# Kernel tuning notes

Measured on AMD Instinct MI355X. Metric: run time of the kernel, lower is better.

Reference implementation:

```python
import jax, jax.numpy as jnp
import numpy as np
import math

B, S, N, F = 512, 72, 5, 10
H, C = 4, 32          # GAT heads, per-head dim
D = H * C             # 128 d_model
L, FF = 3, 256        # transformer layers, ffn dim
K, NS = 6, 5          # horizons, stations
EPS = 1e-5


def layer_norm(x, g, b):
    m = x.mean(-1, keepdims=True)
    v = ((x - m) ** 2).mean(-1, keepdims=True)
    return (x - m) / jnp.sqrt(v + EPS) * g + b


def setup_inputs() -> dict:
    key = jax.random.key(0)
    ks = jax.random.split(key, 16)
    # all 20 directed non-self edges of the 5-node graph
    src, dst = np.nonzero(1 - np.eye(N, dtype=np.int32))
    edge_index = jnp.asarray(np.stack([src, dst]).astype(np.int32))
    w = lambda k, shp: (jax.random.normal(k, shp, jnp.float32) * 0.05)
    return {
        "x": jax.random.normal(ks[0], (B, S, N, F), jnp.float32),
        "edge_index": edge_index,
        "gat_w": w(ks[1], (F, D)),
        "gat_att_src": w(ks[2], (H, C)),
        "gat_att_dst": w(ks[3], (H, C)),
        "gat_bias": jnp.zeros((D,), jnp.float32),
        "gat_ln_g": jnp.ones((D,), jnp.float32),
        "gat_ln_b": jnp.zeros((D,), jnp.float32),
        "qkv_w": w(ks[4], (L, 3 * D, D)),
        "qkv_b": jnp.zeros((L, 3 * D), jnp.float32),
        "out_w": w(ks[5], (L, D, D)),
        "out_b": jnp.zeros((L, D), jnp.float32),
        "ln1_g": jnp.ones((L, D), jnp.float32),
        "ln1_b": jnp.zeros((L, D), jnp.float32),
        "ff1_w": w(ks[6], (L, FF, D)),
        "ff1_b": jnp.zeros((L, FF), jnp.float32),
        "ff2_w": w(ks[7], (L, D, FF)),
        "ff2_b": jnp.zeros((L, D), jnp.float32),
        "ln2_g": jnp.ones((L, D), jnp.float32),
        "ln2_b": jnp.zeros((L, D), jnp.float32),
        "h1_w": w(ks[8], (K, D // 2, D)),
        "h1_b": jnp.zeros((K, D // 2), jnp.float32),
        "h2_w": w(ks[9], (K, NS, D // 2)),
        "h2_b": jnp.zeros((K, NS), jnp.float32),
    }


def reference(x, edge_index, gat_w, gat_att_src, gat_att_dst, gat_bias,
              gat_ln_g, gat_ln_b, qkv_w, qkv_b, out_w, out_b,
              ln1_g, ln1_b, ff1_w, ff1_b, ff2_w, ff2_b, ln2_g, ln2_b,
              h1_w, h1_b, h2_w, h2_b):
    G = B * S                                  # number of independent graphs
    xf = x.reshape(G, N, F)
    # GATConv: per-node projection then edge-softmax attention per destination
    h = jnp.einsum('gnf,fhc->gnhc', xf, gat_w.reshape(F, H, C))   # [G,N,H,C]
    a_src = jnp.einsum('gnhc,hc->gnh', h, gat_att_src)
    a_dst = jnp.einsum('gnhc,hc->gnh', h, gat_att_dst)
    # add self loops (GATConv default; input has no self loops)
    loops = jnp.arange(N, dtype=edge_index.dtype)
    src = jnp.concatenate([edge_index[0], loops])   # [E2]
    dst = jnp.concatenate([edge_index[1], loops])
    e = jax.nn.leaky_relu(a_src[:, src] + a_dst[:, dst], 0.2)     # [G,E2,H]
    et = e.transpose(1, 0, 2)                                     # [E2,G,H]
    m = jax.ops.segment_max(et, dst, num_segments=N)              # [N,G,H]
    ex = jnp.exp(et - m[dst])
    denom = jax.ops.segment_sum(ex, dst, num_segments=N)          # [N,G,H]
    alpha = ex / denom[dst]                                       # [E2,G,H]
    msg = alpha[..., None] * h[:, src].transpose(1, 0, 2, 3)      # [E2,G,H,C]
    agg = jax.ops.segment_sum(msg, dst, num_segments=N)           # [N,G,H,C]
    gat_out = agg.transpose(1, 0, 2, 3).reshape(G, N, D) + gat_bias
    gat_out = layer_norm(gat_out, gat_ln_g, gat_ln_b)

    # mean-pool over nodes -> temporal sequence [B,S,D]
    t = gat_out.reshape(B, S, N, D).mean(axis=2)

    # sinusoidal positional encoding
    pos = jnp.arange(S, dtype=jnp.float32)[:, None]
    div = jnp.exp(jnp.arange(0, D, 2, dtype=jnp.float32) * (-math.log(10000.0) / D))
    pe = jnp.zeros((S, D), jnp.float32)
    pe = pe.at[:, 0::2].set(jnp.sin(pos * div)).at[:, 1::2].set(jnp.cos(pos * div))
    t = t + pe

    scale = 1.0 / math.sqrt(D // H)
    for l in range(L):
        qkv = t @ qkv_w[l].T + qkv_b[l]                 # [B,S,3D]
        q, k, v = jnp.split(qkv, 3, axis=-1)
        q = q.reshape(B, S, H, D // H)
        k = k.reshape(B, S, H, D // H)
        v = v.reshape(B, S, H, D // H)
        scores = jnp.einsum('bqhd,bkhd->bhqk', q, k) * scale
        att = jax.nn.softmax(scores, axis=-1)
        o = jnp.einsum('bhqk,bkhd->bqhd', att, v).reshape(B, S, D)
        o = o @ out_w[l].T + out_b[l]
        t = layer_norm(t + o, ln1_g[l], ln1_b[l])       # post-norm
        f = jax.nn.relu(t @ ff1_w[l].T + ff1_b[l]) @ ff2_w[l].T + ff2_b[l]
        t = layer_norm(t + f, ln2_g[l], ln2_b[l])

    x_last = t[:, -1, :]                                # [B,D]
    h1 = jax.nn.relu(jnp.einsum('bd,kod->kbo', x_last, h1_w) + h1_b[:, None, :])
    out = jnp.einsum('kbo,kpo->kbp', h1, h2_w) + h2_b[:, None, :]
    return out  # [K=6 horizons, B, NS=5]
```

## Files before the change

### kernel.cpp

```cpp
#include <hip/hip_runtime.h>
#include <math.h>

constexpr int B_ = 512, S_ = 72, N_ = 5, F_ = 10;
constexpr int H_ = 4, C_ = 32, D_ = 128;
constexpr int L_ = 3, FF_ = 256;
constexpr int K_ = 6, NS_ = 5;
constexpr int G_ = B_ * S_;
constexpr float EPS_ = 1e-5f;
constexpr int SP_ = 80;
constexpr int KP_ = 96;

typedef short bf16x8 __attribute__((ext_vector_type(8)));
typedef float f32x4 __attribute__((ext_vector_type(4)));

__device__ __forceinline__ short f2bf(float f) {
    unsigned int u = __float_as_uint(f);
    u += 0x7FFFu + ((u >> 16) & 1u);
    return (short)(u >> 16);
}

__global__ __launch_bounds__(128) void pe_kernel(float* __restrict__ pe)
{
    const int s = blockIdx.x;
    const int d = threadIdx.x;
    const float expo = -(float)(d & ~1) * (9.210340371976184f / 128.f);
    const float ang = (float)s * expf(expo);
    pe[s * D_ + d] = (d & 1) ? cosf(ang) : sinf(ang);
}

__global__ __launch_bounds__(128) void gatc_kernel(
    const float* __restrict__ gat_w, const float* __restrict__ att_src,
    const float* __restrict__ att_dst, float* __restrict__ gatc)
{
    const int t = threadIdx.x;
    if (t < 40) {
        const int f = t >> 2, h = t & 3;
        float s = 0.f;
#pragma unroll
        for (int c = 0; c < 32; ++c)
            s = fmaf(gat_w[f * D_ + h * 32 + c], att_src[h * 32 + c], s);
        gatc[t] = s;
    } else if (t < 80) {
        const int f = (t - 40) >> 2, h = (t - 40) & 3;
        float s = 0.f;
#pragma unroll
        for (int c = 0; c < 32; ++c)
            s = fmaf(gat_w[f * D_ + h * 32 + c], att_dst[h * 32 + c], s);
        gatc[t] = s;
    }
}

__global__ __launch_bounds__(128) void gat_kernel(
    const float* __restrict__ x,
    const float* __restrict__ gat_w,
    const float* __restrict__ gatc,
    const float* __restrict__ gat_bias,
    const float* __restrict__ ln_g,
    const float* __restrict__ ln_b,
    const float* __restrict__ pe,
    float* __restrict__ t_out)
{
    const int g = blockIdx.x;
    const int d = threadIdx.x;
    const int s = g % S_;
    const int head = d >> 5;

    __shared__ float xs[N_][F_];
    __shared__ float red[N_][2][2];

    if (d < N_ * F_) xs[d / F_][d % F_] = x[(size_t)g * N_ * F_ + d];
    __syncthreads();

    float wcol[F_], wsrcv[F_], wdstv[F_];
#pragma unroll
    for (int f = 0; f < F_; ++f) {
        wcol[f]  = gat_w[f * D_ + d];
        wsrcv[f] = gatc[f * 4 + head];
        wdstv[f] = gatc[40 + f * 4 + head];
    }

    float hn[N_], a_s[N_], a_d[N_];
#pragma unroll
    for (int n = 0; n < N_; ++n) {
        float acc = 0.f, ss = 0.f, dd = 0.f;
#pragma unroll
        for (int f = 0; f < F_; ++f) {
            const float xv = xs[n][f];
            acc = fmaf(xv, wcol[f], acc);
            ss  = fmaf(xv, wsrcv[f], ss);
            dd  = fmaf(xv, wdstv[f], dd);
        }
        hn[n] = acc; a_s[n] = ss; a_d[n] = dd;
    }

    float y[N_];
#pragma unroll
    for (int n = 0; n < N_; ++n) {
        const float ad = a_d[n];
        float e[N_];
        float mx = -1e30f;
#pragma unroll
        for (int m = 0; m < N_; ++m) {
            float v = a_s[m] + ad;
            v = v > 0.f ? v : 0.2f * v;
            e[m] = v;
            mx = fmaxf(mx, v);
        }
        float den = 0.f;
#pragma unroll
        for (int m = 0; m < N_; ++m) { e[m] = __expf(e[m] - mx); den += e[m]; }
        const float inv = 1.f / den;
        float agg = 0.f;
#pragma unroll
        for (int m = 0; m < N_; ++m) agg = fmaf(e[m] * inv, hn[m], agg);
        y[n] = agg + gat_bias[d];
    }

    const int wave = d >> 6;
#pragma unroll
    for (int n = 0; n < N_; ++n) {
        float sm = y[n];
        float sq = y[n] * y[n];
#pragma unroll
        for (int off = 32; off >= 1; off >>= 1) {
            sm += __shfl_xor(sm, off);
            sq += __shfl_xor(sq, off);
        }
        if ((d & 63) == 0) { red[n][wave][0] = sm; red[n][wave][1] = sq; }
    }
    __syncthreads();

    const float gg = ln_g[d];
    const float bb = ln_b[d];
    float tacc = 0.f;
#pragma unroll
    for (int n = 0; n < N_; ++n) {
        const float sm = red[n][0][0] + red[n][1][0];
        const float sq = red[n][0][1] + red[n][1][1];
        const float mean = sm * (1.f / D_);
        const float var = sq * (1.f / D_) - mean * mean;
        const float rstd = rsqrtf(var + EPS_);
        tacc += (y[n] - mean) * rstd * gg + bb;
    }
    tacc *= (1.f / N_);

    t_out[(size_t)g * D_ + d] = tacc + pe[s * D_ + d];
}

__global__ __launch_bounds__(256) void linear_mfma_kernel(
    const float* __restrict__ A, const float* __restrict__ W,
    const float* __restrict__ bias, float* __restrict__ out,
    int K, int Cout, int relu)
{
    __shared__ short As[64 * 64];
    __shared__ short Ws[64 * 64];

    const int tid = threadIdx.x;
    const int lane = tid & 63;
    const int wid = tid >> 6;
    const int wr = wid >> 1;
    const int wc = wid & 1;
    const int r0 = blockIdx.x * 64;
    const int c0 = blockIdx.y * 64;

    const int st_row = tid >> 3;
    const int st_slot = tid & 7;

    f32x4 acc[2][2] = {};

    for (int kk = 0; kk < K; kk += 64) {
        if (kk) __syncthreads();
#pragma unroll
        for (int it = 0; it < 2; ++it) {
            const int row = st_row + it * 32;
            const int gk = kk + st_slot * 8;
            const int pslot = st_slot ^ (row & 7);
            {
                const float* src = &A[(size_t)(r0 + row) * K + gk];
                const float4 a0 = *reinterpret_cast<const float4*>(src);
                const float4 a1 = *reinterpret_cast<const float4*>(src + 4);
                bf16x8 h;
                h[0] = f2bf(a0.x); h[1] = f2bf(a0.y);
                h[2] = f2bf(a0.z); h[3] = f2bf(a0.w);
                h[4] = f2bf(a1.x); h[5] = f2bf(a1.y);
                h[6] = f2bf(a1.z); h[7] = f2bf(a1.w);
                *reinterpret_cast<bf16x8*>(&As[row * 64 + pslot * 8]) = h;
            }
            {
                const float* src = &W[(size_t)(c0 + row) * K + gk];
                const float4 w0 = *reinterpret_cast<const float4*>(src);
                const float4 w1 = *reinterpret_cast<const float4*>(src + 4);
                bf16x8 h;
                h[0] = f2bf(w0.x); h[1] = f2bf(w0.y);
                h[2] = f2bf(w0.z); h[3] = f2bf(w0.w);
                h[4] = f2bf(w1.x); h[5] = f2bf(w1.y);
                h[6] = f2bf(w1.z); h[7] = f2bf(w1.w);
                *reinterpret_cast<bf16x8*>(&Ws[row * 64 + pslot * 8]) = h;
            }
        }
        __syncthreads();

#pragma unroll
        for (int j = 0; j < 2; ++j) {
            bf16x8 aF[2], bF[2];
#pragma unroll
            for (int m = 0; m < 2; ++m) {
                const int row = wr * 32 + m * 16 + (lane & 15);
                const int slot = j * 4 + (lane >> 4);
                const int pslot = slot ^ (row & 7);
                aF[m] = *reinterpret_cast<const bf16x8*>(&As[row * 64 + pslot * 8]);
            }
#pragma unroll
            for (int n = 0; n < 2; ++n) {
                const int col = wc * 32 + n * 16 + (lane & 15);
                const int slot = j * 4 + (lane >> 4);
                const int pslot = slot ^ (col & 7);
                bF[n] = *reinterpret_cast<const bf16x8*>(&Ws[col * 64 + pslot * 8]);
            }
#pragma unroll
            for (int m = 0; m < 2; ++m)
#pragma unroll
                for (int n = 0; n < 2; ++n)
                    acc[m][n] = __builtin_amdgcn_mfma_f32_16x16x32_bf16(
                        aF[m], bF[n], acc[m][n], 0, 0, 0);
        }
    }

#pragma unroll
    for (int m = 0; m < 2; ++m) {
#pragma unroll
        for (int n = 0; n < 2; ++n) {
            const int col = c0 + wc * 32 + n * 16 + (lane & 15);
            const float bv = bias[col];
#pragma unroll
            for (int j = 0; j < 4; ++j) {
                const int row = r0 + wr * 32 + m * 16 + (lane >> 4) * 4 + j;
                float v = acc[m][n][j] + bv;
                if (relu) v = fmaxf(v, 0.f);
                out[(size_t)row * Cout + col] = v;
            }
        }
    }
}

__global__ __launch_bounds__(256) void linear_ln_kernel(
    const float* __restrict__ A, const float* __restrict__ W,
    const float* __restrict__ bias, float* __restrict__ t,
    const float* __restrict__ lng, const float* __restrict__ lnb,
    int K)
{
    __shared__ short As[64 * 64];
    __shared__ short Ws2[128 * 64];
    __shared__ float red[64][2][2];

    const int tid = threadIdx.x;
    const int lane = tid & 63;
    const int wid = tid >> 6;
    const int wr = wid >> 1;
    const int wc = wid & 1;
    const int c16 = lane & 15;
    const int grp = lane >> 4;
    const int r0 = blockIdx.x * 64;

    const int st_row = tid >> 3;
    const int st_slot = tid & 7;

    f32x4 acc[2][4] = {};

    for (int kk = 0; kk < K; kk += 64) {
        if (kk) __syncthreads();
#pragma unroll
        for (int it = 0; it < 2; ++it) {
            const int row = st_row + it * 32;
            const int gk = kk + st_slot * 8;
            const int pslot = st_slot ^ (row & 7);
            const float* src = &A[(size_t)(r0 + row) * K + gk];
            const float4 a0 = *reinterpret_cast<const float4*>(src);
            const float4 a1 = *reinterpret_cast<const float4*>(src + 4);
            bf16x8 h;
            h[0] = f2bf(a0.x); h[1] = f2bf(a0.y);
            h[2] = f2bf(a0.z); h[3] = f2bf(a0.w);
            h[4] = f2bf(a1.x); h[5] = f2bf(a1.y);
            h[6] = f2bf(a1.z); h[7] = f2bf(a1.w);
            *reinterpret_cast<bf16x8*>(&As[row * 64 + pslot * 8]) = h;
        }
#pragma unroll
        for (int it = 0; it < 4; ++it) {
            const int row = st_row + it * 32;
            const int gk = kk + st_slot * 8;
            const int pslot = st_slot ^ (row & 7);
            const float* src = &W[(size_t)row * K + gk];
            const float4 w0 = *reinterpret_cast<const float4*>(src);
            const float4 w1 = *reinterpret_cast<const float4*>(src + 4);
            bf16x8 h;
            h[0] = f2bf(w0.x); h[1] = f2bf(w0.y);
            h[2] = f2bf(w0.z); h[3] = f2bf(w0.w);
            h[4] = f2bf(w1.x); h[5] = f2bf(w1.y);
            h[6] = f2bf(w1.z); h[7] = f2bf(w1.w);
            *reinterpret_cast<bf16x8*>(&Ws2[row * 64 + pslot * 8]) = h;
        }
        __syncthreads();

#pragma unroll
        for (int j = 0; j < 2; ++j) {
            bf16x8 aF[2], bF[4];
#pragma unroll
            for (int m = 0; m < 2; ++m) {
                const int row = wr * 32 + m * 16 + c16;
                const int slot = j * 4 + grp;
                const int pslot = slot ^ (row & 7);
                aF[m] = *reinterpret_cast<const bf16x8*>(&As[row * 64 + pslot * 8]);
            }
#pragma unroll
            for (int n = 0; n < 4; ++n) {
                const int col = wc * 64 + n * 16 + c16;
                const int slot = j * 4 + grp;
                const int pslot = slot ^ (col & 7);
                bF[n] = *reinterpret_cast<const bf16x8*>(&Ws2[col * 64 + pslot * 8]);
            }
#pragma unroll
            for (int m = 0; m < 2; ++m)
#pragma unroll
                for (int n = 0; n < 4; ++n)
                    acc[m][n] = __builtin_amdgcn_mfma_f32_16x16x32_bf16(
                        aF[m], bF[n], acc[m][n], 0, 0, 0);
        }
    }

#pragma unroll
    for (int m = 0; m < 2; ++m) {
#pragma unroll
        for (int j = 0; j < 4; ++j) {
            const int row = wr * 32 + m * 16 + 4 * grp + j;
            float sm = 0.f, sq = 0.f;
#pragma unroll
            for (int n = 0; n < 4; ++n) {
                const int col = wc * 64 + n * 16 + c16;
                float v = acc[m][n][j] + bias[col]
                        + t[(size_t)(r0 + row) * D_ + col];
                acc[m][n][j] = v;
                sm += v;
                sq += v * v;
            }
#pragma unroll
            for (int off = 8; off >= 1; off >>= 1) {
                sm += __shfl_xor(sm, off);
                sq += __shfl_xor(sq, off);
            }
            if (c16 == 0) { red[row][wc][0] = sm; red[row][wc][1] = sq; }
        }
    }
    __syncthreads();

#pragma unroll
    for (int m = 0; m < 2; ++m) {
#pragma unroll
        for (int j = 0; j < 4; ++j) {
            const int row = wr * 32 + m * 16 + 4 * grp + j;
            const float sm = red[row][0][0] + red[row][1][0];
            const float sq = red[row][0][1] + red[row][1][1];
            const float mean = sm * (1.f / D_);
            const float var = sq * (1.f / D_) - mean * mean;
            const float rstd = rsqrtf(var + EPS_);
#pragma unroll
            for (int n = 0; n < 4; ++n) {
                const int col = wc * 64 + n * 16 + c16;
                t[(size_t)(r0 + row) * D_ + col] =
                    (acc[m][n][j] - mean) * rstd * lng[col] + lnb[col];
            }
        }
    }
}

__global__ __launch_bounds__(256) void attn_mfma_kernel(
    const float* __restrict__ qkv, float* __restrict__ o)
{
    const int bh = blockIdx.x;
    const int b = bh >> 2;
    const int h = bh & 3;

    __shared__ short Qs[SP_ * 32];
    __shared__ short Ks[SP_ * 32];
    __shared__ short VT[32 * KP_];
    __shared__ short Pb[SP_ * KP_];

    const int tid = threadIdx.x;
    const int lane = tid & 63;
    const int wid = tid >> 6;
    const int g = lane >> 4;
    const int c16 = lane & 15;

    const float scale = 0.17677669529663687f;

    for (int idx = tid; idx < S_ * 8; idx += 256) {
        const int i = idx >> 3;
        const int c4 = (idx & 7) * 4;
        const size_t base = ((size_t)(b * S_ + i)) * 384 + h * 32 + c4;
        const float4 q = *reinterpret_cast<const float4*>(&qkv[base]);
        const float4 k = *reinterpret_cast<const float4*>(&qkv[base + 128]);
        const float4 v = *reinterpret_cast<const float4*>(&qkv[base + 256]);
        short4 qh, kh;
        qh.x = f2bf(q.x * scale); qh.y = f2bf(q.y * scale);
        qh.z = f2bf(q.z * scale); qh.w = f2bf(q.w * scale);
        kh.x = f2bf(k.x); kh.y = f2bf(k.y);
        kh.z = f2bf(k.z); kh.w = f2bf(k.w);
        *reinterpret_cast<short4*>(&Qs[i * 32 + c4]) = qh;
        *reinterpret_cast<short4*>(&Ks[i * 32 + c4]) = kh;
        VT[(c4 + 0) * KP_ + i] = f2bf(v.x);
        VT[(c4 + 1) * KP_ + i] = f2bf(v.y);
        VT[(c4 + 2) * KP_ + i] = f2bf(v.z);
        VT[(c4 + 3) * KP_ + i] = f2bf(v.w);
    }
    for (int idx = tid; idx < 8 * 32; idx += 256) {
        Qs[S_ * 32 + idx] = 0;
        Ks[S_ * 32 + idx] = 0;
    }
    for (int idx = tid; idx < 32 * 24; idx += 256) {
        VT[(idx / 24) * KP_ + 72 + idx % 24] = 0;
    }
    for (int idx = tid; idx < SP_ * 24; idx += 256) {
        Pb[(idx / 24) * KP_ + 72 + idx % 24] = 0;
    }
    __syncthreads();

    float invr[2][4];
#pragma unroll
    for (int mi = 0; mi < 2; ++mi) {
        const int m = wid + 4 * mi;
        if (m <= 4) {
            const int rowb = m * 16;
            const bf16x8 aF = *reinterpret_cast<const bf16x8*>(
                &Qs[(rowb + c16) * 32 + 8 * g]);
            f32x4 sc[5];
#pragma unroll
            for (int n = 0; n < 5; ++n) {
                const bf16x8 bF = *reinterpret_cast<const bf16x8*>(
                    &Ks[(n * 16 + c16) * 32 + 8 * g]);
                f32x4 z = {};
                sc[n] = __builtin_amdgcn_mfma_f32_16x16x32_bf16(aF, bF, z, 0, 0, 0);
            }
#pragma unroll
            for (int j = 0; j < 4; ++j) {
                float mx = -1e30f;
#pragma unroll
                for (int n = 0; n < 5; ++n) {
                    const int col = n * 16 + c16;
                    if (col < S_) mx = fmaxf(mx, sc[n][j]);
                }
                mx = fmaxf(mx, __shfl_xor(mx, 1));
                mx = fmaxf(mx, __shfl_xor(mx, 2));
                mx = fmaxf(mx, __shfl_xor(mx, 4));
                mx = fmaxf(mx, __shfl_xor(mx, 8));
                float den = 0.f;
                float p[5];
#pragma unroll
                for (int n = 0; n < 5; ++n) {
                    const int col = n * 16 + c16;
                    p[n] = (col < S_) ? __expf(sc[n][j] - mx) : 0.f;
                    den += p[n];
                }
                den += __shfl_xor(den, 1);
                den += __shfl_xor(den, 2);
                den += __shfl_xor(den, 4);
                den += __shfl_xor(den, 8);
                invr[mi][j] = 1.f / den;
                const int row = rowb + 4 * g + j;
#pragma unroll
                for (int n = 0; n < 5; ++n)
                    Pb[row * KP_ + n * 16 + c16] = f2bf(p[n]);
            }
        }
    }
    __syncthreads();

#pragma unroll
    for (int mi = 0; mi < 2; ++mi) {
        const int m = wid + 4 * mi;
        if (m <= 4) {
            const int rowb = m * 16;
            f32x4 accO[2] = {};
#pragma unroll
            for (int kk = 0; kk < 3; ++kk) {
                const bf16x8 aF = *reinterpret_cast<const bf16x8*>(
                    &Pb[(rowb + c16) * KP_ + kk * 32 + 8 * g]);
#pragma unroll
                for (int n2 = 0; n2 < 2; ++n2) {
                    const bf16x8 bF = *reinterpret_cast<const bf16x8*>(
                        &VT[(n2 * 16 + c16) * KP_ + kk * 32 + 8 * g]);
                    accO[n2] = __builtin_amdgcn_mfma_f32_16x16x32_bf16(
                        aF, bF, accO[n2], 0, 0, 0);
                }
            }
#pragma unroll
            for (int j = 0; j < 4; ++j) {
                const int row = rowb + 4 * g + j;
                if (row < S_) {
                    const float inv = invr[mi][j];
#pragma unroll
                    for (int n2 = 0; n2 < 2; ++n2) {
                        o[((size_t)(b * S_ + row)) * D_ + h * 32 + n2 * 16 + c16]
                            = accO[n2][j] * inv;
                    }
                }
            }
        }
    }
}

__global__ __launch_bounds__(64) void head_kernel(
    const float* __restrict__ t, const float* __restrict__ h1_w,
    const float* __restrict__ h1_b, const float* __restrict__ h2_w,
    const float* __restrict__ h2_b, float* __restrict__ out)
{
    const int kb = blockIdx.x;
    const int k = kb / B_;
    const int b = kb - k * B_;
    const int o = threadIdx.x;

    const float* xr = &t[((size_t)(b * S_ + S_ - 1)) * D_];
    const float* wr = &h1_w[((size_t)k * 64 + o) * D_];
    float acc = h1_b[k * 64 + o];
#pragma unroll 8
    for (int d = 0; d < D_; ++d) acc = fmaf(xr[d], wr[d], acc);
    const float h1v = fmaxf(acc, 0.f);

#pragma unroll
    for (int p = 0; p < NS_; ++p) {
        float partial = h1v * h2_w[((size_t)k * NS_ + p) * 64 + o];
#pragma unroll
        for (int off = 32; off >= 1; off >>= 1) partial += __shfl_xor(partial, off);
        if (o == 0) out[((size_t)k * B_ + b) * NS_ + p] = partial + h2_b[k * NS_ + p];
    }
}

extern "C" void kernel_launch(void* const* d_in, const int* in_sizes, int n_in,
                              void* d_out, int out_size, void* d_ws, size_t ws_size,
                              hipStream_t stream) {
    const float* x        = (const float*)d_in[0];
    const float* gat_w    = (const float*)d_in[2];
    const float* att_src  = (const float*)d_in[3];
    const float* att_dst  = (const float*)d_in[4];
    const float* gat_bias = (const float*)d_in[5];
    const float* gat_ln_g = (const float*)d_in[6];
    const float* gat_ln_b = (const float*)d_in[7];
    const float* qkv_w    = (const float*)d_in[8];
    const float* qkv_b    = (const float*)d_in[9];
    const float* out_w    = (const float*)d_in[10];
    const float* out_b    = (const float*)d_in[11];
    const float* ln1_g    = (const float*)d_in[12];
    const float* ln1_b    = (const float*)d_in[13];
    const float* ff1_w    = (const float*)d_in[14];
    const float* ff1_b    = (const float*)d_in[15];
    const float* ff2_w    = (const float*)d_in[16];
    const float* ff2_b    = (const float*)d_in[17];
    const float* ln2_g    = (const float*)d_in[18];
    const float* ln2_b    = (const float*)d_in[19];
    const float* h1_w     = (const float*)d_in[20];
    const float* h1_b     = (const float*)d_in[21];
    const float* h2_w     = (const float*)d_in[22];
    const float* h2_b     = (const float*)d_in[23];
    float* out = (float*)d_out;

    float* ws   = (float*)d_ws;
    float* t    = ws;
    float* qkv  = t + (size_t)G_ * D_;
    float* fbuf = qkv + (size_t)G_ * 384;
    float* pe   = fbuf + (size_t)G_ * FF_;
    float* gatc = pe + (size_t)S_ * D_;

    pe_kernel<<<S_, 128, 0, stream>>>(pe);
    gatc_kernel<<<1, 128, 0, stream>>>(gat_w, att_src, att_dst, gatc);
    gat_kernel<<<G_, 128, 0, stream>>>(x, gat_w, gatc,
                                       gat_bias, gat_ln_g, gat_ln_b, pe, t);

    for (int l = 0; l < L_; ++l) {
        linear_mfma_kernel<<<dim3(G_ / 64, 384 / 64), 256, 0, stream>>>(
            t, qkv_w + (size_t)l * 384 * D_, qkv_b + (size_t)l * 384, qkv,
            D_, 384, 0);
        attn_mfma_kernel<<<B_ * H_, 256, 0, stream>>>(qkv, fbuf);
        linear_ln_kernel<<<G_ / 64, 256, 0, stream>>>(
            fbuf, out_w + (size_t)l * D_ * D_, out_b + (size_t)l * D_, t,
            ln1_g + l * D_, ln1_b + l * D_, D_);
        linear_mfma_kernel<<<dim3(G_ / 64, FF_ / 64), 256, 0, stream>>>(
            t, ff1_w + (size_t)l * FF_ * D_, ff1_b + (size_t)l * FF_, fbuf,
            D_, FF_, 1);
        linear_ln_kernel<<<G_ / 64, 256, 0, stream>>>(
            fbuf, ff2_w + (size_t)l * D_ * FF_, ff2_b + (size_t)l * D_, t,
            ln2_g + l * D_, ln2_b + l * D_, FF_);
    }

    head_kernel<<<K_ * B_, 64, 0, stream>>>(t, h1_w, h1_b, h2_w, h2_b, out);
}
```

Baseline: 470.2 us.

## Store intermediate activations and weights in bf16 to halve memory traffic

Weights are converted to bf16 once per call in a new kernel, and every intermediate activation buffer (qkv, attention output, ffn hidden, plus a bf16 shadow of t) is written in bf16. The GEMM and attention kernels then load bf16 directly instead of loading fp32 and converting per tile. This cuts global memory traffic and conversion ALU work across all layers. It adds an extra bf16 write of t after each layernorm, and rounding now happens before the bias and scale are applied, which slightly changes numerics.

```diff
diff --git a/kernel.cpp b/kernel.cpp
--- a/kernel.cpp
+++ b/kernel.cpp
@@ -10,6 +10,12 @@
 constexpr int SP_ = 80;
 constexpr int KP_ = 96;
 
+constexpr int WQKV_ = 0;
+constexpr int WOUT_ = 147456;
+constexpr int WFF1_ = 196608;
+constexpr int WFF2_ = 294912;
+constexpr int WTOT_ = 393216;
+
 typedef short bf16x8 __attribute__((ext_vector_type(8)));
 typedef float f32x4 __attribute__((ext_vector_type(4)));
 
@@ -48,6 +54,23 @@
             s = fmaf(gat_w[f * D_ + h * 32 + c], att_dst[h * 32 + c], s);
         gatc[t] = s;
     }
+}
+
+__global__ __launch_bounds__(256) void wcvt_kernel(
+    const float* __restrict__ qw, const float* __restrict__ ow,
+    const float* __restrict__ f1, const float* __restrict__ f2,
+    short* __restrict__ wb)
+{
+    const int i4 = (blockIdx.x * 256 + threadIdx.x) * 4;
+    const float* src; int off;
+    if (i4 < WOUT_)      { src = qw; off = i4; }
+    else if (i4 < WFF1_) { src = ow; off = i4 - WOUT_; }
+    else if (i4 < WFF2_) { src = f1; off = i4 - WFF1_; }
+    else                 { src = f2; off = i4 - WFF2_; }
+    const float4 v = *reinterpret_cast<const float4*>(&src[off]);
+    short4 h;
+    h.x = f2bf(v.x); h.y = f2bf(v.y); h.z = f2bf(v.z); h.w = f2bf(v.w);
+    *reinterpret_cast<short4*>(&wb[i4]) = h;
 }
 
 __global__ __launch_bounds__(128) void gat_kernel(
@@ -58,7 +81,8 @@
     const float* __restrict__ ln_g,
     const float* __restrict__ ln_b,
     const float* __restrict__ pe,
-    float* __restrict__ t_out)
+    float* __restrict__ t_out,
+    short* __restrict__ tb_out)
 {
     const int g = blockIdx.x;
     const int d = threadIdx.x;
@@ -144,12 +168,14 @@
     }
     tacc *= (1.f / N_);
 
-    t_out[(size_t)g * D_ + d] = tacc + pe[s * D_ + d];
+    const float val = tacc + pe[s * D_ + d];
+    t_out[(size_t)g * D_ + d] = val;
+    tb_out[(size_t)g * D_ + d] = f2bf(val);
 }
 
 __global__ __launch_bounds__(256) void linear_mfma_kernel(
-    const float* __restrict__ A, const float* __restrict__ W,
-    const float* __restrict__ bias, float* __restrict__ out,
+    const short* __restrict__ A, const short* __restrict__ W,
+    const float* __restrict__ bias, short* __restrict__ out,
     int K, int Cout, int relu)
 {
     __shared__ short As[64 * 64];
@@ -175,28 +201,10 @@
             const int row = st_row + it * 32;
             const int gk = kk + st_slot * 8;
             const int pslot = st_slot ^ (row & 7);
-            {
-                const float* src = &A[(size_t)(r0 + row) * K + gk];
-                const float4 a0 = *reinterpret_cast<const float4*>(src);
-                const float4 a1 = *reinterpret_cast<const float4*>(src + 4);
-                bf16x8 h;
-                h[0] = f2bf(a0.x); h[1] = f2bf(a0.y);
-                h[2] = f2bf(a0.z); h[3] = f2bf(a0.w);
-                h[4] = f2bf(a1.x); h[5] = f2bf(a1.y);
-                h[6] = f2bf(a1.z); h[7] = f2bf(a1.w);
-                *reinterpret_cast<bf16x8*>(&As[row * 64 + pslot * 8]) = h;
-            }
-            {
-                const float* src = &W[(size_t)(c0 + row) * K + gk];
-                const float4 w0 = *reinterpret_cast<const float4*>(src);
-                const float4 w1 = *reinterpret_cast<const float4*>(src + 4);
-                bf16x8 h;
-                h[0] = f2bf(w0.x); h[1] = f2bf(w0.y);
-                h[2] = f2bf(w0.z); h[3] = f2bf(w0.w);
-                h[4] = f2bf(w1.x); h[5] = f2bf(w1.y);
-                h[6] = f2bf(w1.z); h[7] = f2bf(w1.w);
-                *reinterpret_cast<bf16x8*>(&Ws[row * 64 + pslot * 8]) = h;
-            }
+            *reinterpret_cast<bf16x8*>(&As[row * 64 + pslot * 8]) =
+                *reinterpret_cast<const bf16x8*>(&A[(size_t)(r0 + row) * K + gk]);
+            *reinterpret_cast<bf16x8*>(&Ws[row * 64 + pslot * 8]) =
+                *reinterpret_cast<const bf16x8*>(&W[(size_t)(c0 + row) * K + gk]);
         }
         __syncthreads();
 
@@ -237,15 +245,16 @@
                 const int row = r0 + wr * 32 + m * 16 + (lane >> 4) * 4 + j;
                 float v = acc[m][n][j] + bv;
                 if (relu) v = fmaxf(v, 0.f);
-                out[(size_t)row * Cout + col] = v;
+                out[(size_t)row * Cout + col] = f2bf(v);
             }
         }
     }
 }
 
 __global__ __launch_bounds__(256) void linear_ln_kernel(
-    const float* __restrict__ A, const float* __restrict__ W,
+    const short* __restrict__ A, const short* __restrict__ W,
     const float* __restrict__ bias, float* __restrict__ t,
+    short* __restrict__ tb,
     const float* __restrict__ lng, const float* __restrict__ lnb,
     int K)
 {
@@ -274,30 +283,16 @@
             const int row = st_row + it * 32;
             const int gk = kk + st_slot * 8;
             const int pslot = st_slot ^ (row & 7);
-            const float* src = &A[(size_t)(r0 + row) * K + gk];
-            const float4 a0 = *reinterpret_cast<const float4*>(src);
-            const float4 a1 = *reinterpret_cast<const float4*>(src + 4);
-            bf16x8 h;
-            h[0] = f2bf(a0.x); h[1] = f2bf(a0.y);
-            h[2] = f2bf(a0.z); h[3] = f2bf(a0.w);
-            h[4] = f2bf(a1.x); h[5] = f2bf(a1.y);
-            h[6] = f2bf(a1.z); h[7] = f2bf(a1.w);
-            *reinterpret_cast<bf16x8*>(&As[row * 64 + pslot * 8]) = h;
+            *reinterpret_cast<bf16x8*>(&As[row * 64 + pslot * 8]) =
+                *reinterpret_cast<const bf16x8*>(&A[(size_t)(r0 + row) * K + gk]);
         }
 #pragma unroll
         for (int it = 0; it < 4; ++it) {
             const int row = st_row + it * 32;
             const int gk = kk + st_slot * 8;
             const int pslot = st_slot ^ (row & 7);
-            const float* src = &W[(size_t)row * K + gk];
-            const float4 w0 = *reinterpret_cast<const float4*>(src);
-            const float4 w1 = *reinterpret_cast<const float4*>(src + 4);
-            bf16x8 h;
-            h[0] = f2bf(w0.x); h[1] = f2bf(w0.y);
-            h[2] = f2bf(w0.z); h[3] = f2bf(w0.w);
-            h[4] = f2bf(w1.x); h[5] = f2bf(w1.y);
-            h[6] = f2bf(w1.z); h[7] = f2bf(w1.w);
-            *reinterpret_cast<bf16x8*>(&Ws2[row * 64 + pslot * 8]) = h;
+            *reinterpret_cast<bf16x8*>(&Ws2[row * 64 + pslot * 8]) =
+                *reinterpret_cast<const bf16x8*>(&W[(size_t)row * K + gk]);
         }
         __syncthreads();
 
@@ -365,15 +360,16 @@
 #pragma unroll
             for (int n = 0; n < 4; ++n) {
                 const int col = wc * 64 + n * 16 + c16;
-                t[(size_t)(r0 + row) * D_ + col] =
-                    (acc[m][n][j] - mean) * rstd * lng[col] + lnb[col];
+                const float o = (acc[m][n][j] - mean) * rstd * lng[col] + lnb[col];
+                t[(size_t)(r0 + row) * D_ + col] = o;
+                tb[(size_t)(r0 + row) * D_ + col] = f2bf(o);
             }
         }
     }
 }
 
 __global__ __launch_bounds__(256) void attn_mfma_kernel(
-    const float* __restrict__ qkv, float* __restrict__ o)
+    const short* __restrict__ qkv, short* __restrict__ o)
 {
     const int bh = blockIdx.x;
     const int b = bh >> 2;
@@ -392,24 +388,17 @@
 
     const float scale = 0.17677669529663687f;
 
-    for (int idx = tid; idx < S_ * 8; idx += 256) {
-        const int i = idx >> 3;
-        const int c4 = (idx & 7) * 4;
-        const size_t base = ((size_t)(b * S_ + i)) * 384 + h * 32 + c4;
-        const float4 q = *reinterpret_cast<const float4*>(&qkv[base]);
-        const float4 k = *reinterpret_cast<const float4*>(&qkv[base + 128]);
-        const float4 v = *reinterpret_cast<const float4*>(&qkv[base + 256]);
-        short4 qh, kh;
-        qh.x = f2bf(q.x * scale); qh.y = f2bf(q.y * scale);
-        qh.z = f2bf(q.z * scale); qh.w = f2bf(q.w * scale);
-        kh.x = f2bf(k.x); kh.y = f2bf(k.y);
-        kh.z = f2bf(k.z); kh.w = f2bf(k.w);
-        *reinterpret_cast<short4*>(&Qs[i * 32 + c4]) = qh;
-        *reinterpret_cast<short4*>(&Ks[i * 32 + c4]) = kh;
-        VT[(c4 + 0) * KP_ + i] = f2bf(v.x);
-        VT[(c4 + 1) * KP_ + i] = f2bf(v.y);
-        VT[(c4 + 2) * KP_ + i] = f2bf(v.z);
-        VT[(c4 + 3) * KP_ + i] = f2bf(v.w);
+    for (int idx = tid; idx < S_ * 4; idx += 256) {
+        const int i = idx >> 2;
+        const int c8 = (idx & 3) * 8;
+        const size_t base = ((size_t)(b * S_ + i)) * 384 + h * 32 + c8;
+        const bf16x8 q = *reinterpret_cast<const bf16x8*>(&qkv[base]);
+        const bf16x8 k = *reinterpret_cast<const bf16x8*>(&qkv[base + 128]);
+        const bf16x8 v = *reinterpret_cast<const bf16x8*>(&qkv[base + 256]);
+        *reinterpret_cast<bf16x8*>(&Qs[i * 32 + c8]) = q;
+        *reinterpret_cast<bf16x8*>(&Ks[i * 32 + c8]) = k;
+#pragma unroll
+        for (int j = 0; j < 8; ++j) VT[(c8 + j) * KP_ + i] = v[j];
     }
     for (int idx = tid; idx < 8 * 32; idx += 256) {
         Qs[S_ * 32 + idx] = 0;
@@ -438,6 +427,7 @@
                     &Ks[(n * 16 + c16) * 32 + 8 * g]);
                 f32x4 z = {};
                 sc[n] = __builtin_amdgcn_mfma_f32_16x16x32_bf16(aF, bF, z, 0, 0, 0);
+                sc[n] = sc[n] * scale;
             }
 #pragma unroll
             for (int j = 0; j < 4; ++j) {
@@ -499,7 +489,7 @@
 #pragma unroll
                     for (int n2 = 0; n2 < 2; ++n2) {
                         o[((size_t)(b * S_ + row)) * D_ + h * 32 + n2 * 16 + c16]
-                            = accO[n2][j] * inv;
+                            = f2bf(accO[n2][j] * inv);
                     }
                 }
             }
@@ -561,31 +551,39 @@
     const float* h2_b     = (const float*)d_in[23];
     float* out = (float*)d_out;
 
-    float* ws   = (float*)d_ws;
-    float* t    = ws;
-    float* qkv  = t + (size_t)G_ * D_;
-    float* fbuf = qkv + (size_t)G_ * 384;
-    float* pe   = fbuf + (size_t)G_ * FF_;
-    float* gatc = pe + (size_t)S_ * D_;
+    float* base = (float*)d_ws;
+    float* t     = base;               base += (size_t)G_ * D_;
+    short* qkvb  = (short*)base;       base += (size_t)G_ * 192;
+    short* fbufb = (short*)base;       base += (size_t)G_ * 128;
+    short* tb    = (short*)base;       base += (size_t)G_ * 64;
+    float* pe    = base;               base += (size_t)S_ * D_;
+    float* gatc  = base;               base += 128;
+    short* wb    = (short*)base;
 
     pe_kernel<<<S_, 128, 0, stream>>>(pe);
     gatc_kernel<<<1, 128, 0, stream>>>(gat_w, att_src, att_dst, gatc);
+    wcvt_kernel<<<WTOT_ / 1024, 256, 0, stream>>>(qkv_w, out_w, ff1_w, ff2_w, wb);
     gat_kernel<<<G_, 128, 0, stream>>>(x, gat_w, gatc,
-                                       gat_bias, gat_ln_g, gat_ln_b, pe, t);
+                                       gat_bias, gat_ln_g, gat_ln_b, pe, t, tb);
+
+    const short* wq = wb + WQKV_;
+    const short* wo = wb + WOUT_;
+    const short* w1 = wb + WFF1_;
+    const short* w2 = wb + WFF2_;
 
     for (int l = 0; l < L_; ++l) {
         linear_mfma_kernel<<<dim3(G_ / 64, 384 / 64), 256, 0, stream>>>(
-            t, qkv_w + (size_t)l * 384 * D_, qkv_b + (size_t)l * 384, qkv,
+            tb, wq + (size_t)l * 384 * D_, qkv_b + (size_t)l * 384, qkvb,
             D_, 384, 0);
-        attn_mfma_kernel<<<B_ * H_, 256, 0, stream>>>(qkv, fbuf);
+        attn_mfma_kernel<<<B_ * H_, 256, 0, stream>>>(qkvb, fbufb);
         linear_ln_kernel<<<G_ / 64, 256, 0, stream>>>(
-            fbuf, out_w + (size_t)l * D_ * D_, out_b + (size_t)l * D_, t,
+            fbufb, wo + (size_t)l * D_ * D_, out_b + (size_t)l * D_, t, tb,
             ln1_g + l * D_, ln1_b + l * D_, D_);
         linear_mfma_kernel<<<dim3(G_ / 64, FF_ / 64), 256, 0, stream>>>(
-            t, ff1_w + (size_t)l * FF_ * D_, ff1_b + (size_t)l * FF_, fbuf,
+            tb, w1 + (size_t)l * FF_ * D_, ff1_b + (size_t)l * FF_, fbufb,
             D_, FF_, 1);
         linear_ln_kernel<<<G_ / 64, 256, 0, stream>>>(
-            fbuf, ff2_w + (size_t)l * D_ * FF_, ff2_b + (size_t)l * D_, t,
+            fbufb, w2 + (size_t)l * D_ * FF_, ff2_b + (size_t)l * D_, t, tb,
             ln2_g + l * D_, ln2_b + l * D_, FF_);
     }
 
```

New measurement: 418.6 us. 1.12x faster.
